# Kernel tuning notes

Measured on AMD Instinct MI355X. Metric: run time of the kernel, lower is better.

## Reference

```python
import jax, jax.numpy as jnp
import numpy as np

N, K, D_LOCAL, P, BINS = 8192, 32, 256, 128, 64
N_RBF, REL_CLIP = 16, 32
REL_DIM = 2 * REL_CLIP + 2  # 65 rel-pos buckets + 1 'different chain/batch' bucket
N_ATOMS = 5


def _normalize(v, eps=1e-8):
    return v / (jnp.linalg.norm(v, axis=-1, keepdims=True) + eps)


def _frames(pos):
    # Gram-Schmidt backbone frames from N, CA, C atoms. pos: [N, A, 3]
    n, ca, c = pos[:, 0], pos[:, 1], pos[:, 2]
    e1 = _normalize(c - ca)
    v2 = n - ca
    e2 = _normalize(v2 - jnp.sum(v2 * e1, -1, keepdims=True) * e1)
    e3 = jnp.cross(e1, e2)
    return jnp.stack([e1, e2, e3], axis=-1)  # [N, 3, 3], columns are basis


def setup_inputs() -> dict:
    key = jax.random.key(0)
    ks = jax.random.split(key, 16)
    inp = {
        "local": jax.random.normal(ks[0], (N, D_LOCAL), jnp.float32),
        "pos": jax.random.normal(ks[1], (N, N_ATOMS, 3), jnp.float32) * 3.0,
        "neighbours": jax.random.randint(ks[2], (N, K), 0, N, jnp.int32),
        "resi": jnp.arange(N, dtype=jnp.int32),
        "chain": jnp.zeros((N,), jnp.int32),
        "batch": jnp.zeros((N,), jnp.int32),
        "mask": jnp.ones((N,), bool),
    }
    def lin(k, fan_in, fan_out):
        return jax.random.normal(k, (fan_in, fan_out), jnp.float32) / np.sqrt(fan_in)
    inp["W_relpos"] = lin(ks[3], REL_DIM, P)
    inp["W_dist"] = lin(ks[4], N_RBF, P)
    inp["W_dir"] = lin(ks[5], 3, P)
    inp["W_rot"] = lin(ks[6], 9, P)
    inp["W_pvec"] = lin(ks[7], N_ATOMS * 3, P)
    inp["W_loc_i"] = lin(ks[8], D_LOCAL, P)
    inp["W_loc_j"] = lin(ks[9], D_LOCAL, P)
    inp["ln_scale"] = jnp.ones((P,), jnp.float32)
    inp["ln_bias"] = jnp.zeros((P,), jnp.float32)
    inp["W1"] = lin(ks[10], P, 2 * P)
    inp["b1"] = jnp.zeros((2 * P,), jnp.float32)
    inp["W2"] = lin(ks[11], 2 * P, BINS) * 0.02  # final layer (small init; zeros in original)
    inp["b2"] = jnp.zeros((BINS,), jnp.float32)
    return inp


def reference(local, pos, neighbours, resi, chain, batch, mask,
              W_relpos, W_dist, W_dir, W_rot, W_pvec, W_loc_i, W_loc_j,
              ln_scale, ln_bias, W1, b1, W2, b2):
    idx = jnp.where(neighbours < 0, 0, neighbours)          # safe gather index [N, K]
    m = mask.astype(jnp.float32)
    pair_mask = m[:, None] * m[idx] * (neighbours != -1)    # [N, K]

    # --- sequence relative position (one-hot, clipped to +/-32) ---
    rel = jnp.clip(resi[idx] - resi[:, None], -REL_CLIP, REL_CLIP) + REL_CLIP
    same = (chain[:, None] == chain[idx]) & (batch[:, None] == batch[idx])
    code = jnp.where(same, rel, REL_DIM - 1)
    f_rel = jax.nn.one_hot(code, REL_DIM, dtype=jnp.float32)  # [N, K, 66]

    # --- geometric features ---
    ca = pos[:, 1]                                           # [N, 3]
    R = _frames(pos)                                         # [N, 3, 3]
    dvec = ca[idx] - ca[:, None]                             # [N, K, 3]
    d = jnp.linalg.norm(dvec, axis=-1)                       # [N, K]
    centers = jnp.linspace(0.0, 22.0, N_RBF)
    sigma = 22.0 / N_RBF
    f_dist = jnp.exp(-((d[..., None] - centers) ** 2) / (2 * sigma ** 2))  # [N,K,16]
    unit = dvec / (d[..., None] + 1e-8)
    f_dir = jnp.einsum("nab,nka->nkb", R, unit)              # [N, K, 3] direction in local frame
    f_rot = jnp.einsum("nab,nkac->nkbc", R, R[idx]).reshape(d.shape + (9,))  # R_i^T R_j
    pv = pos[idx] - ca[:, None, None]                        # [N, K, A, 3]
    f_pv = jnp.einsum("nab,nkma->nkmb", R, pv).reshape(d.shape + (N_ATOMS * 3,))

    # --- multi-branch linear fusion ---
    pair = (f_rel @ W_relpos + f_dist @ W_dist + f_dir @ W_dir
            + f_rot @ W_rot + f_pv @ W_pvec
            + (local @ W_loc_i)[:, None] + (local @ W_loc_j)[idx])
    pair = pair * pair_mask[..., None]

    # --- LayerNorm (create_scale/offset, eps=1e-5) ---
    mu = jnp.mean(pair, axis=-1, keepdims=True)
    var = jnp.mean((pair - mu) ** 2, axis=-1, keepdims=True)
    pair = (pair - mu) * jax.lax.rsqrt(var + 1e-5) * ln_scale + ln_bias

    # --- MLP + log_softmax ---
    hidden = jax.nn.gelu(pair @ W1 + b1)
    distogram = hidden @ W2 + b2                             # [N, K, 64]
    return jax.nn.log_softmax(distogram, axis=-1)
```

## Files before the change

### kernel.cpp

```cpp
#include <hip/hip_runtime.h>
#include <hip/hip_bf16.h>
#include <math.h>

#define N_NODES 8192
#define KNBR    32
#define PDIM    128
#define BINS    64
#define REL_CLIP 32
#define REL_DIM  66

typedef unsigned short ushort_t;
typedef short v8s  __attribute__((ext_vector_type(8)));
typedef float v4f  __attribute__((ext_vector_type(4)));

__device__ __forceinline__ ushort_t f2bf(float f) {
    union { __hip_bfloat16 b; ushort_t u; } cv;
    cv.b = __float2bfloat16(f);
    return cv.u;
}
__device__ __forceinline__ unsigned int pk2bf(float lo, float hiv) {
    union { __hip_bfloat162 h2; unsigned int u; } cv;
    cv.h2 = __float22bfloat162_rn(make_float2(lo, hiv));
    return cv.u;
}
__device__ __forceinline__ float gelu_sig(float x) {
    float e = exp2f(-2.4554045f * x);
    return x / (1.f + e);
}

__global__ __launch_bounds__(256) void prep_kernel(
    const float* __restrict__ W_dist, const float* __restrict__ W_dir,
    const float* __restrict__ W_rot, const float* __restrict__ W_pvec,
    const float* __restrict__ W_relpos,
    const float* __restrict__ W1, const float* __restrict__ W2,
    const float* __restrict__ W_loc_i, const float* __restrict__ W_loc_j,
    const float* __restrict__ ln_scale, const float* __restrict__ ln_bias,
    const float* __restrict__ b1,
    ushort_t* __restrict__ Wcomb, ushort_t* __restrict__ W1Ts,
    ushort_t* __restrict__ W2T, ushort_t* __restrict__ W_locT,
    float* __restrict__ b1p)
{
    int idx = blockIdx.x * 256 + threadIdx.x;
    if (idx < 16384) {
        int col = idx >> 7, k = idx & 127;
        float v = 0.f;
        if (k < 16)       v = W_dist[k * PDIM + col];
        else if (k < 19)  v = W_dir[(k - 16) * PDIM + col];
        else if (k < 28)  v = W_rot[(k - 19) * PDIM + col];
        else if (k < 43)  v = W_pvec[(k - 28) * PDIM + col];
        else if (k < 109) v = W_relpos[(size_t)(k - 43) * PDIM + col];
        Wcomb[idx] = f2bf(v);
    } else if (idx < 49152) {
        int o = idx - 16384;
        int col = o >> 7, k = o & 127;
        W1Ts[o] = f2bf(W1[(size_t)k * 256 + col] * ln_scale[k]);
    } else if (idx < 65536) {
        int o = idx - 49152;
        int col = o >> 8, k = o & 255;
        W2T[o] = f2bf(W2[(size_t)k * BINS + col]);
    } else if (idx < 131072) {
        int o = idx - 65536;
        int oc = o >> 8, k = o & 255;
        float v = (oc < 128) ? W_loc_i[(size_t)k * 128 + oc]
                             : W_loc_j[(size_t)k * 128 + (oc - 128)];
        W_locT[o] = f2bf(v);
    } else if (idx < 131328) {
        int c = idx - 131072;
        float s = b1[c];
        for (int k = 0; k < 128; ++k) s += ln_bias[k] * W1[(size_t)k * 256 + c];
        b1p[c] = s;
    }
}

__global__ __launch_bounds__(256) void locframe_kernel(
    const float* __restrict__ local, const float* __restrict__ pos,
    const ushort_t* __restrict__ W_locT,
    float* __restrict__ R_ws, float* __restrict__ loci_ws, float* __restrict__ locj_ws)
{
    __shared__ __align__(16) ushort_t LB[32 * 264];
    const int tid = threadIdx.x;
    const int base = blockIdx.x * 32;
    const int wid = tid >> 6, lane = tid & 63, c15 = lane & 15, hi = lane >> 4;

    if (tid < 32) {
        const int n = base + tid;
        const float* pp = pos + (size_t)n * 15;
        float nx = pp[0], ny = pp[1], nz = pp[2];
        float cax = pp[3], cay = pp[4], caz = pp[5];
        float cx = pp[6], cy = pp[7], cz = pp[8];
        float e1x = cx - cax, e1y = cy - cay, e1z = cz - caz;
        float n1 = sqrtf(e1x*e1x + e1y*e1y + e1z*e1z) + 1e-8f;
        e1x /= n1; e1y /= n1; e1z /= n1;
        float v2x = nx - cax, v2y = ny - cay, v2z = nz - caz;
        float dp = v2x*e1x + v2y*e1y + v2z*e1z;
        float wx = v2x - dp*e1x, wy = v2y - dp*e1y, wz = v2z - dp*e1z;
        float n2 = sqrtf(wx*wx + wy*wy + wz*wz) + 1e-8f;
        float e2x = wx/n2, e2y = wy/n2, e2z = wz/n2;
        float4 f0, f1, f2;
        f0.x = e1x; f0.y = e1y; f0.z = e1z; f0.w = e2x;
        f1.x = e2y; f1.y = e2z;
        f1.z = e1y*e2z - e1z*e2y;
        f1.w = e1z*e2x - e1x*e2z;
        f2.x = e1x*e2y - e1y*e2x;
        f2.y = 0.f; f2.z = 0.f; f2.w = 0.f;
        float* R = R_ws + (size_t)n * 12;
        *(float4*)&R[0] = f0;
        *(float4*)&R[4] = f1;
        *(float4*)&R[8] = f2;
    }
    #pragma unroll
    for (int it = 0; it < 8; ++it) {
        int f = tid + it * 256;
        int row = f >> 6, kc = f & 63;
        float4 L = *(const float4*)&local[((size_t)(base + row)) * 256 + kc * 4];
        uint2 w8; w8.x = pk2bf(L.x, L.y); w8.y = pk2bf(L.z, L.w);
        *(uint2*)&LB[row * 264 + kc * 4] = w8;
    }
    __syncthreads();

    v4f acc[4][2];
    #pragma unroll
    for (int a = 0; a < 4; ++a)
        #pragma unroll
        for (int b = 0; b < 2; ++b) { acc[a][b][0]=0.f; acc[a][b][1]=0.f; acc[a][b][2]=0.f; acc[a][b][3]=0.f; }
    #pragma unroll
    for (int ks = 0; ks < 8; ++ks) {
        v8s bF[2];
        #pragma unroll
        for (int bt = 0; bt < 2; ++bt)
            bF[bt] = *(const v8s*)&LB[(bt*16 + c15) * 264 + ks*32 + hi*8];
        #pragma unroll
        for (int act = 0; act < 4; ++act) {
            v8s aF = *(const v8s*)&W_locT[(size_t)(wid*64 + act*16 + c15) * 256 + ks*32 + hi*8];
            #pragma unroll
            for (int bt = 0; bt < 2; ++bt)
                acc[act][bt] = __builtin_amdgcn_mfma_f32_16x16x32_bf16(aF, bF[bt], acc[act][bt], 0, 0, 0);
        }
    }
    #pragma unroll
    for (int act = 0; act < 4; ++act) {
        const int oc0 = wid*64 + act*16 + hi*4;
        #pragma unroll
        for (int bt = 0; bt < 2; ++bt) {
            const int lrow = bt*16 + c15;
            float4 v;
            v.x = acc[act][bt][0]; v.y = acc[act][bt][1];
            v.z = acc[act][bt][2]; v.w = acc[act][bt][3];
            if (oc0 < 128)
                *(float4*)&loci_ws[(size_t)(base + lrow) * 128 + oc0] = v;
            else
                *(float4*)&locj_ws[(size_t)(base + lrow) * 128 + (oc0 - 128)] = v;
        }
    }
}

__device__ __forceinline__ void loadR(const float* __restrict__ R_ws, int n, float* Ri) {
    float4 f0 = *(const float4*)&R_ws[(size_t)n * 12 + 0];
    float4 f1 = *(const float4*)&R_ws[(size_t)n * 12 + 4];
    float4 f2 = *(const float4*)&R_ws[(size_t)n * 12 + 8];
    Ri[0] = f0.x; Ri[1] = f0.y; Ri[2] = f0.z;
    Ri[3] = f0.w; Ri[4] = f1.x; Ri[5] = f1.y;
    Ri[6] = f1.z; Ri[7] = f1.w; Ri[8] = f2.x;
}

__global__ __launch_bounds__(256, 4) void pair_kernel(
    const float* __restrict__ pos, const int* __restrict__ neighbours,
    const int* __restrict__ resi, const int* __restrict__ chain,
    const int* __restrict__ batch, const int* __restrict__ mask,
    const float* __restrict__ b1p, const float* __restrict__ b2,
    const float* __restrict__ R_ws, const float* __restrict__ loci_ws,
    const float* __restrict__ locj_ws,
    const ushort_t* __restrict__ Wcomb, const ushort_t* __restrict__ W1Ts,
    const ushort_t* __restrict__ W2T, float* __restrict__ out)
{
    __shared__ __align__(16) ushort_t SH0[64 * 128];
    __shared__ __align__(16) ushort_t HT[64 * 128];
    float2* redLN = (float2*)HT;
    float*  redSM = (float*)SH0;

    const int tid = threadIdx.x;
    const int ib = blockIdx.x;
    const int base = ib * 2;
    const int wid = tid >> 6, lane = tid & 63, c15 = lane & 15, hi = lane >> 4;
    const int brow = wid * 16 + c15;
    const int sw = c15 & 7;

    int nbv[4], jv[4];
    #pragma unroll
    for (int bt = 0; bt < 4; ++bt) {
        const int rr = bt * 16 + c15;
        nbv[bt] = neighbours[(size_t)(base + (bt >> 1)) * KNBR + (rr & 31)];
        jv[bt] = nbv[bt] < 0 ? 0 : nbv[bt];
    }
    const int node_own = base + (wid >> 1);
    const int j_own = wid == 0 ? jv[0] : wid == 1 ? jv[1] : wid == 2 ? jv[2] : jv[3];

    {
        int rel = resi[j_own] - resi[node_own];
        rel = rel < -REL_CLIP ? -REL_CLIP : (rel > REL_CLIP ? REL_CLIP : rel);
        rel += REL_CLIP;
        const int code = ((chain[j_own] == chain[node_own]) && (batch[j_own] == batch[node_own]))
                         ? rel : (REL_DIM - 1);
        float Ri[9];
        loadR(R_ws, node_own, Ri);
        const float cax = pos[(size_t)node_own*15 + 3], cay = pos[(size_t)node_own*15 + 4], caz = pos[(size_t)node_own*15 + 5];
        const float* pj = pos + (size_t)j_own * 15;
        const float dx = pj[3] - cax, dy = pj[4] - cay, dz = pj[5] - caz;

        v8s featF[4];
        #pragma unroll
        for (int ks = 1; ks < 4; ++ks) {
            const int cb = ks*32 + hi*8 - 43;
            v8s v;
            #pragma unroll
            for (int t = 0; t < 8; ++t) v[t] = (short)((code == cb + t) ? 0x3F80 : 0);
            featF[ks] = v;
        }
        #define DOTR(b,X,Y,Z) (Ri[(b)*3]*(X) + Ri[(b)*3+1]*(Y) + Ri[(b)*3+2]*(Z))
        const float d = sqrtf(dx*dx + dy*dy + dz*dz);
        if (hi == 0) {
            v8s v;
            #pragma unroll
            for (int r = 0; r < 8; ++r) { float dd = d - (22.f/15.f)*r; v[r] = (short)f2bf(__expf(-dd*dd*(1.f/3.78125f))); }
            featF[0] = v;
            float p2x = pj[6]-cax, p2y = pj[7]-cay, p2z = pj[8]-caz;
            float p3x = pj[9]-cax, p3y = pj[10]-cay, p3z = pj[11]-caz;
            v8s w;
            w[0] = (short)f2bf(DOTR(1, dx, dy, dz));
            w[1] = (short)f2bf(DOTR(2, dx, dy, dz));
            w[2] = (short)f2bf(DOTR(0, p2x, p2y, p2z));
            w[3] = (short)f2bf(DOTR(1, p2x, p2y, p2z));
            w[4] = (short)f2bf(DOTR(2, p2x, p2y, p2z));
            w[5] = (short)f2bf(DOTR(0, p3x, p3y, p3z));
            w[6] = (short)f2bf(DOTR(1, p3x, p3y, p3z));
            w[7] = (short)f2bf(DOTR(2, p3x, p3y, p3z));
            featF[1] = w;
        } else if (hi == 1) {
            v8s v;
            #pragma unroll
            for (int r = 0; r < 8; ++r) { float dd = d - (22.f/15.f)*(r+8); v[r] = (short)f2bf(__expf(-dd*dd*(1.f/3.78125f))); }
            featF[0] = v;
            float p4x = pj[12]-cax, p4y = pj[13]-cay, p4z = pj[14]-caz;
            v8s w = featF[1];
            w[0] = (short)f2bf(DOTR(0, p4x, p4y, p4z));
            w[1] = (short)f2bf(DOTR(1, p4x, p4y, p4z));
            w[2] = (short)f2bf(DOTR(2, p4x, p4y, p4z));
            featF[1] = w;
        } else if (hi == 2) {
            float inv = 1.f / (d + 1e-8f);
            float ux = dx*inv, uy = dy*inv, uz = dz*inv;
            float Rj[9];
            loadR(R_ws, j_own, Rj);
            #define ROT(b,c) (Ri[(b)*3]*Rj[(c)*3] + Ri[(b)*3+1]*Rj[(c)*3+1] + Ri[(b)*3+2]*Rj[(c)*3+2])
            v8s v;
            v[0] = (short)f2bf(DOTR(0, ux, uy, uz));
            v[1] = (short)f2bf(DOTR(1, ux, uy, uz));
            v[2] = (short)f2bf(DOTR(2, ux, uy, uz));
            v[3] = (short)f2bf(ROT(0,0));
            v[4] = (short)f2bf(ROT(0,1));
            v[5] = (short)f2bf(ROT(0,2));
            v[6] = (short)f2bf(ROT(1,0));
            v[7] = (short)f2bf(ROT(1,1));
            featF[0] = v;
            #undef ROT
        } else {
            float Rj[9];
            loadR(R_ws, j_own, Rj);
            #define ROT(b,c) (Ri[(b)*3]*Rj[(c)*3] + Ri[(b)*3+1]*Rj[(c)*3+1] + Ri[(b)*3+2]*Rj[(c)*3+2])
            float p0x = pj[0]-cax, p0y = pj[1]-cay, p0z = pj[2]-caz;
            v8s v;
            v[0] = (short)f2bf(ROT(1,2));
            v[1] = (short)f2bf(ROT(2,0));
            v[2] = (short)f2bf(ROT(2,1));
            v[3] = (short)f2bf(ROT(2,2));
            v[4] = (short)f2bf(DOTR(0, p0x, p0y, p0z));
            v[5] = (short)f2bf(DOTR(1, p0x, p0y, p0z));
            v[6] = (short)f2bf(DOTR(2, p0x, p0y, p0z));
            v[7] = (short)f2bf(DOTR(0, dx, dy, dz));
            featF[0] = v;
            #undef ROT
        }
        #undef DOTR
        #pragma unroll
        for (int ks = 0; ks < 4; ++ks)
            *(v8s*)&SH0[brow * 128 + (((ks*4 + hi) ^ sw) << 3)] = featF[ks];
    }
    __syncthreads();

    float mu0, mu1, mu2, mu3, rs0, rs1, rs2, rs3;
    {
        v4f pacc[2][4];
        #pragma unroll
        for (int at = 0; at < 2; ++at)
            #pragma unroll
            for (int bt = 0; bt < 4; ++bt) { pacc[at][bt][0]=0.f; pacc[at][bt][1]=0.f; pacc[at][bt][2]=0.f; pacc[at][bt][3]=0.f; }
        #pragma unroll
        for (int ks = 0; ks < 4; ++ks) {
            v8s bF[4];
            #pragma unroll
            for (int bt = 0; bt < 4; ++bt)
                bF[bt] = *(const v8s*)&SH0[(bt*16 + c15) * 128 + (((ks*4 + hi) ^ sw) << 3)];
            #pragma unroll
            for (int at = 0; at < 2; ++at) {
                v8s aF = *(const v8s*)&Wcomb[(size_t)((wid*2 + at)*16 + c15) * 128 + ks*32 + hi*8];
                #pragma unroll
                for (int bt = 0; bt < 4; ++bt)
                    pacc[at][bt] = __builtin_amdgcn_mfma_f32_16x16x32_bf16(aF, bF[bt], pacc[at][bt], 0, 0, 0);
            }
        }
        const int mi0 = mask[base], mi1 = mask[base + 1];
        float pmv[4];
        #pragma unroll
        for (int bt = 0; bt < 4; ++bt) {
            const int min_ = (bt < 2) ? mi0 : mi1;
            pmv[bt] = (min_ != 0 && mask[jv[bt]] != 0 && nbv[bt] != -1) ? 1.f : 0.f;
        }
        float4 liA[2][2], ljA[2][4];
        #pragma unroll
        for (int at = 0; at < 2; ++at) {
            const int ch0 = wid*32 + at*16 + hi*4;
            liA[at][0] = *(const float4*)&loci_ws[(size_t)base * 128 + ch0];
            liA[at][1] = *(const float4*)&loci_ws[(size_t)(base + 1) * 128 + ch0];
            #pragma unroll
            for (int bt = 0; bt < 4; ++bt)
                ljA[at][bt] = *(const float4*)&locj_ws[(size_t)jv[bt] * 128 + ch0];
        }
        float sA[4], qA[4];
        #pragma unroll
        for (int bt = 0; bt < 4; ++bt) {
            float s = 0.f, q = 0.f;
            #pragma unroll
            for (int at = 0; at < 2; ++at) {
                const float4 li = (bt < 2) ? liA[at][0] : liA[at][1];
                const float4 lj = ljA[at][bt];
                float v0 = (pacc[at][bt][0] + li.x + lj.x) * pmv[bt];
                float v1 = (pacc[at][bt][1] + li.y + lj.y) * pmv[bt];
                float v2 = (pacc[at][bt][2] + li.z + lj.z) * pmv[bt];
                float v3 = (pacc[at][bt][3] + li.w + lj.w) * pmv[bt];
                pacc[at][bt][0] = v0; pacc[at][bt][1] = v1; pacc[at][bt][2] = v2; pacc[at][bt][3] = v3;
                s += v0 + v1 + v2 + v3;
                q += v0*v0 + v1*v1 + v2*v2 + v3*v3;
            }
            s += __shfl_xor(s, 16, 64);  q += __shfl_xor(q, 16, 64);
            s += __shfl_xor(s, 32, 64);  q += __shfl_xor(q, 32, 64);
            sA[bt] = s; qA[bt] = q;
        }
        {
            float ssel = hi == 0 ? sA[0] : hi == 1 ? sA[1] : hi == 2 ? sA[2] : sA[3];
            float qsel = hi == 0 ? qA[0] : hi == 1 ? qA[1] : hi == 2 ? qA[2] : qA[3];
            redLN[lane * 5 + wid] = make_float2(ssel, qsel);
        }
        __syncthreads();
        #pragma unroll
        for (int bt = 0; bt < 4; ++bt) {
            const int rr = bt*16 + c15;
            float2 r0 = redLN[rr*5+0], r1 = redLN[rr*5+1], r2 = redLN[rr*5+2], r3 = redLN[rr*5+3];
            float s = r0.x + r1.x + r2.x + r3.x;
            float q = r0.y + r1.y + r2.y + r3.y;
            float mu = s * (1.f/128.f);
            float rs = rsqrtf(q * (1.f/128.f) - mu*mu + 1e-5f);
            if (bt == 0) { mu0 = mu; rs0 = rs; }
            else if (bt == 1) { mu1 = mu; rs1 = rs; }
            else if (bt == 2) { mu2 = mu; rs2 = rs; }
            else { mu3 = mu; rs3 = rs; }
        }
        #pragma unroll
        for (int at = 0; at < 2; ++at) {
            const int chA = (wid*4 + at*2 + (hi >> 1));
            #pragma unroll
            for (int bt = 0; bt < 4; ++bt) {
                const float mu = bt == 0 ? mu0 : bt == 1 ? mu1 : bt == 2 ? mu2 : mu3;
                const float rs = bt == 0 ? rs0 : bt == 1 ? rs1 : bt == 2 ? rs2 : rs3;
                const float nm = -mu * rs;
                float z0 = fmaf(pacc[at][bt][0], rs, nm);
                float z1 = fmaf(pacc[at][bt][1], rs, nm);
                float z2 = fmaf(pacc[at][bt][2], rs, nm);
                float z3 = fmaf(pacc[at][bt][3], rs, nm);
                uint2 w8; w8.x = pk2bf(z0, z1); w8.y = pk2bf(z2, z3);
                const int row = bt*16 + c15;
                *(uint2*)&SH0[row * 128 + ((chA ^ sw) << 3) + (hi & 1) * 4] = w8;
            }
        }
    }
    __syncthreads();

    v4f acc5[4];
    #pragma unroll
    for (int bt = 0; bt < 4; ++bt) { acc5[bt][0]=0.f; acc5[bt][1]=0.f; acc5[bt][2]=0.f; acc5[bt][3]=0.f; }
    #pragma unroll
    for (int half = 0; half < 2; ++half) {
        v4f acc4[2][4];
        #pragma unroll
        for (int at = 0; at < 2; ++at)
            #pragma unroll
            for (int bt = 0; bt < 4; ++bt) { acc4[at][bt][0]=0.f; acc4[at][bt][1]=0.f; acc4[at][bt][2]=0.f; acc4[at][bt][3]=0.f; }
        #pragma unroll
        for (int ks = 0; ks < 4; ++ks) {
            v8s bF[4];
            #pragma unroll
            for (int bt = 0; bt < 4; ++bt)
                bF[bt] = *(const v8s*)&SH0[(bt*16 + c15) * 128 + (((ks*4 + hi) ^ sw) << 3)];
            #pragma unroll
            for (int at = 0; at < 2; ++at) {
                v8s aF = *(const v8s*)&W1Ts[(size_t)(half*128 + wid*32 + at*16 + c15) * 128 + ks*32 + hi*8];
                #pragma unroll
                for (int bt = 0; bt < 4; ++bt)
                    acc4[at][bt] = __builtin_amdgcn_mfma_f32_16x16x32_bf16(aF, bF[bt], acc4[at][bt], 0, 0, 0);
            }
        }
        #pragma unroll
        for (int at = 0; at < 2; ++at) {
            const int h0 = half*128 + wid*32 + at*16 + hi*4;
            const float4 bv = *(const float4*)&b1p[h0];
            const int chA = (wid*4 + at*2 + (hi >> 1));
            #pragma unroll
            for (int bt = 0; bt < 4; ++bt) {
                float g0 = gelu_sig(acc4[at][bt][0] + bv.x);
                float g1 = gelu_sig(acc4[at][bt][1] + bv.y);
                float g2 = gelu_sig(acc4[at][bt][2] + bv.z);
                float g3 = gelu_sig(acc4[at][bt][3] + bv.w);
                uint2 w8; w8.x = pk2bf(g0, g1); w8.y = pk2bf(g2, g3);
                const int row = bt*16 + c15;
                *(uint2*)&HT[row * 128 + ((chA ^ sw) << 3) + (hi & 1) * 4] = w8;
            }
        }
        __syncthreads();
        #pragma unroll
        for (int ks = 0; ks < 4; ++ks) {
            v8s aF = *(const v8s*)&W2T[(size_t)(wid*16 + c15) * 256 + half*128 + ks*32 + hi*8];
            #pragma unroll
            for (int bt = 0; bt < 4; ++bt) {
                v8s bF = *(const v8s*)&HT[(bt*16 + c15) * 128 + (((ks*4 + hi) ^ sw) << 3)];
                acc5[bt] = __builtin_amdgcn_mfma_f32_16x16x32_bf16(aF, bF, acc5[bt], 0, 0, 0);
            }
        }
        if (half == 0) __syncthreads();
    }

    {
        const float4 bv = *(const float4*)&b2[wid*16 + hi*4];
        float sW[4];
        #pragma unroll
        for (int bt = 0; bt < 4; ++bt) {
            acc5[bt][0] += bv.x; acc5[bt][1] += bv.y; acc5[bt][2] += bv.z; acc5[bt][3] += bv.w;
            float s = __expf(acc5[bt][0]) + __expf(acc5[bt][1])
                    + __expf(acc5[bt][2]) + __expf(acc5[bt][3]);
            s += __shfl_xor(s, 16, 64);
            s += __shfl_xor(s, 32, 64);
            sW[bt] = s;
        }
        {
            float ssel = hi == 0 ? sW[0] : hi == 1 ? sW[1] : hi == 2 ? sW[2] : sW[3];
            redSM[lane * 5 + wid] = ssel;
        }
        __syncthreads();
        #pragma unroll
        for (int bt = 0; bt < 4; ++bt) {
            const int rr = bt*16 + c15;
            float S = redSM[rr*5+0] + redSM[rr*5+1] + redSM[rr*5+2] + redSM[rr*5+3];
            const float lz = __logf(S);
            float4 o;
            o.x = acc5[bt][0] - lz; o.y = acc5[bt][1] - lz;
            o.z = acc5[bt][2] - lz; o.w = acc5[bt][3] - lz;
            *(float4*)&out[((size_t)(ib * 64 + rr)) * 64 + wid*16 + hi*4] = o;
        }
    }
}

extern "C" void kernel_launch(void* const* d_in, const int* in_sizes, int n_in,
                              void* d_out, int out_size, void* d_ws, size_t ws_size,
                              hipStream_t stream) {
    (void)in_sizes; (void)n_in; (void)out_size; (void)ws_size;
    const float* local   = (const float*)d_in[0];
    const float* pos     = (const float*)d_in[1];
    const int* neighbours= (const int*)d_in[2];
    const int* resi      = (const int*)d_in[3];
    const int* chain     = (const int*)d_in[4];
    const int* batch     = (const int*)d_in[5];
    const int* mask      = (const int*)d_in[6];
    const float* W_relpos= (const float*)d_in[7];
    const float* W_dist  = (const float*)d_in[8];
    const float* W_dir   = (const float*)d_in[9];
    const float* W_rot   = (const float*)d_in[10];
    const float* W_pvec  = (const float*)d_in[11];
    const float* W_loc_i = (const float*)d_in[12];
    const float* W_loc_j = (const float*)d_in[13];
    const float* ln_scale= (const float*)d_in[14];
    const float* ln_bias = (const float*)d_in[15];
    const float* W1      = (const float*)d_in[16];
    const float* b1      = (const float*)d_in[17];
    const float* W2      = (const float*)d_in[18];
    const float* b2      = (const float*)d_in[19];
    float* out = (float*)d_out;

    float* R_ws    = (float*)d_ws;
    float* loci_ws = R_ws + (size_t)N_NODES * 12;
    float* locj_ws = loci_ws + (size_t)N_NODES * PDIM;
    ushort_t* Wcomb = (ushort_t*)(locj_ws + (size_t)N_NODES * PDIM);
    ushort_t* W1Ts  = Wcomb + 16384;
    ushort_t* W2T   = W1Ts + 32768;
    ushort_t* W_locT= W2T + 16384;
    float* b1p      = (float*)(W_locT + 65536);

    hipLaunchKernelGGL(prep_kernel, dim3(514), dim3(256), 0, stream,
                       W_dist, W_dir, W_rot, W_pvec, W_relpos, W1, W2,
                       W_loc_i, W_loc_j, ln_scale, ln_bias, b1,
                       Wcomb, W1Ts, W2T, W_locT, b1p);
    hipLaunchKernelGGL(locframe_kernel, dim3(N_NODES / 32), dim3(256), 0, stream,
                       local, pos, W_locT, R_ws, loci_ws, locj_ws);
    hipLaunchKernelGGL(pair_kernel, dim3(N_NODES / 2), dim3(256), 0, stream,
                       pos, neighbours, resi, chain, batch, mask, b1p, b2,
                       R_ws, loci_ws, locj_ws, Wcomb, W1Ts, W2T, out);
}
```

Baseline: 146.6 us.

## Pad LDS rows instead of XOR swizzle and split feature build across waves by type

Shared-memory tiles switch from XOR-swizzled 128-element rows to rows padded to 136 elements, which removes the swizzle arithmetic while still avoiding bank conflicts. Feature construction is reorganised so each lane owns one pair row and each wave computes a different feature group (RBF, direction/rotation, atom vectors, one-hot relpos). Before, every lane computed a slice of every row. The one-hot is now written as zero fill plus a single scalar store. This raises LDS use per block, which could reduce occupancy, and it leaves the per-wave work in the feature stage uneven.

```diff
diff --git a/kernel.cpp b/kernel.cpp
--- a/kernel.cpp
+++ b/kernel.cpp
@@ -8,6 +8,7 @@
 #define BINS    64
 #define REL_CLIP 32
 #define REL_DIM  66
+#define RSTR    136
 
 typedef unsigned short ushort_t;
 typedef short v8s  __attribute__((ext_vector_type(8)));
@@ -173,8 +174,8 @@
     const ushort_t* __restrict__ Wcomb, const ushort_t* __restrict__ W1Ts,
     const ushort_t* __restrict__ W2T, float* __restrict__ out)
 {
-    __shared__ __align__(16) ushort_t SH0[64 * 128];
-    __shared__ __align__(16) ushort_t HT[64 * 128];
+    __shared__ __align__(16) ushort_t SH0[64 * RSTR];
+    __shared__ __align__(16) ushort_t HT[64 * RSTR];
     float2* redLN = (float2*)HT;
     float*  redSM = (float*)SH0;
 
@@ -182,8 +183,6 @@
     const int ib = blockIdx.x;
     const int base = ib * 2;
     const int wid = tid >> 6, lane = tid & 63, c15 = lane & 15, hi = lane >> 4;
-    const int brow = wid * 16 + c15;
-    const int sw = c15 & 7;
 
     int nbv[4], jv[4];
     #pragma unroll
@@ -192,98 +191,90 @@
         nbv[bt] = neighbours[(size_t)(base + (bt >> 1)) * KNBR + (rr & 31)];
         jv[bt] = nbv[bt] < 0 ? 0 : nbv[bt];
     }
-    const int node_own = base + (wid >> 1);
-    const int j_own = wid == 0 ? jv[0] : wid == 1 ? jv[1] : wid == 2 ? jv[2] : jv[3];
 
     {
-        int rel = resi[j_own] - resi[node_own];
-        rel = rel < -REL_CLIP ? -REL_CLIP : (rel > REL_CLIP ? REL_CLIP : rel);
-        rel += REL_CLIP;
-        const int code = ((chain[j_own] == chain[node_own]) && (batch[j_own] == batch[node_own]))
-                         ? rel : (REL_DIM - 1);
+        const int row = lane;
+        const int node = base + (row >> 5);
+        const int nb_f = neighbours[(size_t)node * KNBR + (row & 31)];
+        const int jf = nb_f < 0 ? 0 : nb_f;
+        const float cax = pos[(size_t)node*15 + 3], cay = pos[(size_t)node*15 + 4], caz = pos[(size_t)node*15 + 5];
+        const float* pj = pos + (size_t)jf * 15;
+        const float dx = pj[3] - cax, dy = pj[4] - cay, dz = pj[5] - caz;
+        ushort_t* fr = &SH0[row * RSTR];
         float Ri[9];
-        loadR(R_ws, node_own, Ri);
-        const float cax = pos[(size_t)node_own*15 + 3], cay = pos[(size_t)node_own*15 + 4], caz = pos[(size_t)node_own*15 + 5];
-        const float* pj = pos + (size_t)j_own * 15;
-        const float dx = pj[3] - cax, dy = pj[4] - cay, dz = pj[5] - caz;
-
-        v8s featF[4];
-        #pragma unroll
-        for (int ks = 1; ks < 4; ++ks) {
-            const int cb = ks*32 + hi*8 - 43;
+
+        #define DOTR(b,X,Y,Z) (Ri[(b)*3]*(X) + Ri[(b)*3+1]*(Y) + Ri[(b)*3+2]*(Z))
+        if (wid == 0) {
+            const float d = sqrtf(dx*dx + dy*dy + dz*dz);
+            v8s v0, v1;
+            #pragma unroll
+            for (int r = 0; r < 8; ++r) {
+                float a0 = d - (22.f/15.f)*r;        v0[r] = (short)f2bf(__expf(-a0*a0*(1.f/3.78125f)));
+                float a1 = d - (22.f/15.f)*(r + 8);  v1[r] = (short)f2bf(__expf(-a1*a1*(1.f/3.78125f)));
+            }
+            *(v8s*)&fr[0] = v0;
+            *(v8s*)&fr[8] = v1;
+        } else if (wid == 1) {
+            loadR(R_ws, node, Ri);
+            float Rj[9];
+            loadR(R_ws, jf, Rj);
+            const float d = sqrtf(dx*dx + dy*dy + dz*dz);
+            const float inv = 1.f / (d + 1e-8f);
+            const float ux = dx*inv, uy = dy*inv, uz = dz*inv;
+            #define ROT(b,c) (Ri[(b)*3]*Rj[(c)*3] + Ri[(b)*3+1]*Rj[(c)*3+1] + Ri[(b)*3+2]*Rj[(c)*3+2])
+            const float p0x = pj[0]-cax, p0y = pj[1]-cay, p0z = pj[2]-caz;
+            v8s v0, v1;
+            v0[0] = (short)f2bf(DOTR(0, ux, uy, uz));
+            v0[1] = (short)f2bf(DOTR(1, ux, uy, uz));
+            v0[2] = (short)f2bf(DOTR(2, ux, uy, uz));
+            v0[3] = (short)f2bf(ROT(0,0));
+            v0[4] = (short)f2bf(ROT(0,1));
+            v0[5] = (short)f2bf(ROT(0,2));
+            v0[6] = (short)f2bf(ROT(1,0));
+            v0[7] = (short)f2bf(ROT(1,1));
+            v1[0] = (short)f2bf(ROT(1,2));
+            v1[1] = (short)f2bf(ROT(2,0));
+            v1[2] = (short)f2bf(ROT(2,1));
+            v1[3] = (short)f2bf(ROT(2,2));
+            v1[4] = (short)f2bf(DOTR(0, p0x, p0y, p0z));
+            v1[5] = (short)f2bf(DOTR(1, p0x, p0y, p0z));
+            v1[6] = (short)f2bf(DOTR(2, p0x, p0y, p0z));
+            v1[7] = (short)f2bf(DOTR(0, dx, dy, dz));
+            *(v8s*)&fr[16] = v0;
+            *(v8s*)&fr[24] = v1;
+            #undef ROT
+        } else if (wid == 2) {
+            loadR(R_ws, node, Ri);
+            const float p2x = pj[6]-cax, p2y = pj[7]-cay, p2z = pj[8]-caz;
+            const float p3x = pj[9]-cax, p3y = pj[10]-cay, p3z = pj[11]-caz;
             v8s v;
-            #pragma unroll
-            for (int t = 0; t < 8; ++t) v[t] = (short)((code == cb + t) ? 0x3F80 : 0);
-            featF[ks] = v;
-        }
-        #define DOTR(b,X,Y,Z) (Ri[(b)*3]*(X) + Ri[(b)*3+1]*(Y) + Ri[(b)*3+2]*(Z))
-        const float d = sqrtf(dx*dx + dy*dy + dz*dz);
-        if (hi == 0) {
-            v8s v;
-            #pragma unroll
-            for (int r = 0; r < 8; ++r) { float dd = d - (22.f/15.f)*r; v[r] = (short)f2bf(__expf(-dd*dd*(1.f/3.78125f))); }
-            featF[0] = v;
-            float p2x = pj[6]-cax, p2y = pj[7]-cay, p2z = pj[8]-caz;
-            float p3x = pj[9]-cax, p3y = pj[10]-cay, p3z = pj[11]-caz;
-            v8s w;
-            w[0] = (short)f2bf(DOTR(1, dx, dy, dz));
-            w[1] = (short)f2bf(DOTR(2, dx, dy, dz));
-            w[2] = (short)f2bf(DOTR(0, p2x, p2y, p2z));
-            w[3] = (short)f2bf(DOTR(1, p2x, p2y, p2z));
-            w[4] = (short)f2bf(DOTR(2, p2x, p2y, p2z));
-            w[5] = (short)f2bf(DOTR(0, p3x, p3y, p3z));
-            w[6] = (short)f2bf(DOTR(1, p3x, p3y, p3z));
-            w[7] = (short)f2bf(DOTR(2, p3x, p3y, p3z));
-            featF[1] = w;
-        } else if (hi == 1) {
-            v8s v;
-            #pragma unroll
-            for (int r = 0; r < 8; ++r) { float dd = d - (22.f/15.f)*(r+8); v[r] = (short)f2bf(__expf(-dd*dd*(1.f/3.78125f))); }
-            featF[0] = v;
-            float p4x = pj[12]-cax, p4y = pj[13]-cay, p4z = pj[14]-caz;
-            v8s w = featF[1];
-            w[0] = (short)f2bf(DOTR(0, p4x, p4y, p4z));
-            w[1] = (short)f2bf(DOTR(1, p4x, p4y, p4z));
-            w[2] = (short)f2bf(DOTR(2, p4x, p4y, p4z));
-            featF[1] = w;
-        } else if (hi == 2) {
-            float inv = 1.f / (d + 1e-8f);
-            float ux = dx*inv, uy = dy*inv, uz = dz*inv;
-            float Rj[9];
-            loadR(R_ws, j_own, Rj);
-            #define ROT(b,c) (Ri[(b)*3]*Rj[(c)*3] + Ri[(b)*3+1]*Rj[(c)*3+1] + Ri[(b)*3+2]*Rj[(c)*3+2])
-            v8s v;
-            v[0] = (short)f2bf(DOTR(0, ux, uy, uz));
-            v[1] = (short)f2bf(DOTR(1, ux, uy, uz));
-            v[2] = (short)f2bf(DOTR(2, ux, uy, uz));
-            v[3] = (short)f2bf(ROT(0,0));
-            v[4] = (short)f2bf(ROT(0,1));
-            v[5] = (short)f2bf(ROT(0,2));
-            v[6] = (short)f2bf(ROT(1,0));
-            v[7] = (short)f2bf(ROT(1,1));
-            featF[0] = v;
-            #undef ROT
+            v[0] = (short)f2bf(DOTR(1, dx, dy, dz));
+            v[1] = (short)f2bf(DOTR(2, dx, dy, dz));
+            v[2] = (short)f2bf(DOTR(0, p2x, p2y, p2z));
+            v[3] = (short)f2bf(DOTR(1, p2x, p2y, p2z));
+            v[4] = (short)f2bf(DOTR(2, p2x, p2y, p2z));
+            v[5] = (short)f2bf(DOTR(0, p3x, p3y, p3z));
+            v[6] = (short)f2bf(DOTR(1, p3x, p3y, p3z));
+            v[7] = (short)f2bf(DOTR(2, p3x, p3y, p3z));
+            *(v8s*)&fr[32] = v;
         } else {
-            float Rj[9];
-            loadR(R_ws, j_own, Rj);
-            #define ROT(b,c) (Ri[(b)*3]*Rj[(c)*3] + Ri[(b)*3+1]*Rj[(c)*3+1] + Ri[(b)*3+2]*Rj[(c)*3+2])
-            float p0x = pj[0]-cax, p0y = pj[1]-cay, p0z = pj[2]-caz;
-            v8s v;
-            v[0] = (short)f2bf(ROT(1,2));
-            v[1] = (short)f2bf(ROT(2,0));
-            v[2] = (short)f2bf(ROT(2,1));
-            v[3] = (short)f2bf(ROT(2,2));
-            v[4] = (short)f2bf(DOTR(0, p0x, p0y, p0z));
-            v[5] = (short)f2bf(DOTR(1, p0x, p0y, p0z));
-            v[6] = (short)f2bf(DOTR(2, p0x, p0y, p0z));
-            v[7] = (short)f2bf(DOTR(0, dx, dy, dz));
-            featF[0] = v;
-            #undef ROT
+            loadR(R_ws, node, Ri);
+            const float p4x = pj[12]-cax, p4y = pj[13]-cay, p4z = pj[14]-caz;
+            v8s v = {0,0,0,0,0,0,0,0};
+            v[0] = (short)f2bf(DOTR(0, p4x, p4y, p4z));
+            v[1] = (short)f2bf(DOTR(1, p4x, p4y, p4z));
+            v[2] = (short)f2bf(DOTR(2, p4x, p4y, p4z));
+            *(v8s*)&fr[40] = v;
+            const v8s z = {0,0,0,0,0,0,0,0};
+            #pragma unroll
+            for (int c = 6; c < 16; ++c) *(v8s*)&fr[c * 8] = z;
+            int rel = resi[jf] - resi[node];
+            rel = rel < -REL_CLIP ? -REL_CLIP : (rel > REL_CLIP ? REL_CLIP : rel);
+            rel += REL_CLIP;
+            const int code = ((chain[jf] == chain[node]) && (batch[jf] == batch[node])) ? rel : (REL_DIM - 1);
+            fr[43 + code] = (ushort_t)0x3F80;
         }
         #undef DOTR
-        #pragma unroll
-        for (int ks = 0; ks < 4; ++ks)
-            *(v8s*)&SH0[brow * 128 + (((ks*4 + hi) ^ sw) << 3)] = featF[ks];
     }
     __syncthreads();
 
@@ -299,7 +290,7 @@
             v8s bF[4];
             #pragma unroll
             for (int bt = 0; bt < 4; ++bt)
-                bF[bt] = *(const v8s*)&SH0[(bt*16 + c15) * 128 + (((ks*4 + hi) ^ sw) << 3)];
+                bF[bt] = *(const v8s*)&SH0[(bt*16 + c15) * RSTR + (ks*4 + hi) * 8];
             #pragma unroll
             for (int at = 0; at < 2; ++at) {
                 v8s aF = *(const v8s*)&Wcomb[(size_t)((wid*2 + at)*16 + c15) * 128 + ks*32 + hi*8];
@@ -366,7 +357,7 @@
         }
         #pragma unroll
         for (int at = 0; at < 2; ++at) {
-            const int chA = (wid*4 + at*2 + (hi >> 1));
+            const int chA = wid*4 + at*2 + (hi >> 1);
             #pragma unroll
             for (int bt = 0; bt < 4; ++bt) {
                 const float mu = bt == 0 ? mu0 : bt == 1 ? mu1 : bt == 2 ? mu2 : mu3;
@@ -378,7 +369,7 @@
                 float z3 = fmaf(pacc[at][bt][3], rs, nm);
                 uint2 w8; w8.x = pk2bf(z0, z1); w8.y = pk2bf(z2, z3);
                 const int row = bt*16 + c15;
-                *(uint2*)&SH0[row * 128 + ((chA ^ sw) << 3) + (hi & 1) * 4] = w8;
+                *(uint2*)&SH0[row * RSTR + chA * 8 + (hi & 1) * 4] = w8;
             }
         }
     }
@@ -399,7 +390,7 @@
             v8s bF[4];
             #pragma unroll
             for (int bt = 0; bt < 4; ++bt)
-                bF[bt] = *(const v8s*)&SH0[(bt*16 + c15) * 128 + (((ks*4 + hi) ^ sw) << 3)];
+                bF[bt] = *(const v8s*)&SH0[(bt*16 + c15) * RSTR + (ks*4 + hi) * 8];
             #pragma unroll
             for (int at = 0; at < 2; ++at) {
                 v8s aF = *(const v8s*)&W1Ts[(size_t)(half*128 + wid*32 + at*16 + c15) * 128 + ks*32 + hi*8];
@@ -412,7 +403,7 @@
         for (int at = 0; at < 2; ++at) {
             const int h0 = half*128 + wid*32 + at*16 + hi*4;
             const float4 bv = *(const float4*)&b1p[h0];
-            const int chA = (wid*4 + at*2 + (hi >> 1));
+            const int chA = wid*4 + at*2 + (hi >> 1);
             #pragma unroll
             for (int bt = 0; bt < 4; ++bt) {
                 float g0 = gelu_sig(acc4[at][bt][0] + bv.x);
@@ -421,7 +412,7 @@
                 float g3 = gelu_sig(acc4[at][bt][3] + bv.w);
                 uint2 w8; w8.x = pk2bf(g0, g1); w8.y = pk2bf(g2, g3);
                 const int row = bt*16 + c15;
-                *(uint2*)&HT[row * 128 + ((chA ^ sw) << 3) + (hi & 1) * 4] = w8;
+                *(uint2*)&HT[row * RSTR + chA * 8 + (hi & 1) * 4] = w8;
             }
         }
         __syncthreads();
@@ -430,7 +421,7 @@
             v8s aF = *(const v8s*)&W2T[(size_t)(wid*16 + c15) * 256 + half*128 + ks*32 + hi*8];
             #pragma unroll
             for (int bt = 0; bt < 4; ++bt) {
-                v8s bF = *(const v8s*)&HT[(bt*16 + c15) * 128 + (((ks*4 + hi) ^ sw) << 3)];
+                v8s bF = *(const v8s*)&HT[(bt*16 + c15) * RSTR + (ks*4 + hi) * 8];
                 acc5[bt] = __builtin_amdgcn_mfma_f32_16x16x32_bf16(aF, bF, acc5[bt], 0, 0, 0);
             }
         }
```

After: 137.6 us. 1.07x faster.
